# Kernel optimization log

Measured on AMD Instinct MI355X. Metric: run time of the kernel, lower is better.

Reference implementation:

```python
import jax, jax.numpy as jnp
import numpy as np

DIM, HEADS, DIM_HEAD = 1024, 16, 64
INNER = HEADS * DIM_HEAD  # 1024
FF = 4 * DIM
EPS = 1e-5


def layer_norm(x, g, b):
    mu = jnp.mean(x, axis=-1, keepdims=True)
    var = jnp.mean(jnp.square(x - mu), axis=-1, keepdims=True)
    return (x - mu) * jax.lax.rsqrt(var + EPS) * g + b


def setup_inputs() -> dict:
    key = jax.random.key(0)
    ks = jax.random.split(key, 8)
    B, N = 2, 2048
    s = 0.02
    return {
        "x": jax.random.normal(ks[0], (B, N, DIM), dtype=jnp.float32),
        "ln1_g": jnp.ones((DIM,), jnp.float32),
        "ln1_b": jnp.zeros((DIM,), jnp.float32),
        "ln2_g": jnp.ones((DIM,), jnp.float32),
        "ln2_b": jnp.zeros((DIM,), jnp.float32),
        "w_qkv": jax.random.normal(ks[1], (DIM, 3 * INNER), jnp.float32) * s,
        "w_out": jax.random.normal(ks[2], (INNER, DIM), jnp.float32) * s,
        "b_out": jnp.zeros((DIM,), jnp.float32),
        "w_ff1": jax.random.normal(ks[3], (DIM, FF), jnp.float32) * s,
        "b_ff1": jnp.zeros((FF,), jnp.float32),
        "w_ff2": jax.random.normal(ks[4], (FF, DIM), jnp.float32) * s,
        "b_ff2": jnp.zeros((DIM,), jnp.float32),
    }


def reference(x, ln1_g, ln1_b, ln2_g, ln2_b, w_qkv, w_out, b_out,
              w_ff1, b_ff1, w_ff2, b_ff2):
    B, N, _ = x.shape
    scale = DIM_HEAD ** -0.5
    h = layer_norm(x, ln1_g, ln1_b)
    qkv = h @ w_qkv  # [B, N, 3*INNER]
    q, k, v = jnp.split(qkv, 3, axis=-1)
    # b n (h d) -> b h n d
    def to_heads(t):
        return t.reshape(B, N, HEADS, DIM_HEAD).transpose(0, 2, 1, 3)
    q, k, v = to_heads(q), to_heads(k), to_heads(v)
    dots = jnp.einsum('bhnd,bhmd->bhnm', q, k) * scale
    attn = jax.nn.softmax(dots, axis=-1)  # dropout = identity (eval)
    out = jnp.einsum('bhnm,bhmd->bhnd', attn, v)
    out = out.transpose(0, 2, 1, 3).reshape(B, N, INNER)
    out = out @ w_out + b_out
    x = x + out  # residual
    h2 = layer_norm(x, ln2_g, ln2_b)
    ff = jax.nn.gelu(h2 @ w_ff1 + b_ff1, approximate=False) @ w_ff2 + b_ff2
    return x + ff
```

## Files before the change

### kernel.cpp

```cpp
#include <hip/hip_runtime.h>
#include <hip/hip_bf16.h>
#include <math.h>

#define SEQ   2048
#define BATCH 2
#define NROWS 4096
#define DIMM  1024
#define QKV3  3072
#define FFD   4096
#define NHEAD 16
#define DHEAD 64

typedef __bf16 bf16;
typedef __bf16 bf16x4 __attribute__((ext_vector_type(4)));
typedef __bf16 bf16x8 __attribute__((ext_vector_type(8)));
typedef float  f32x4  __attribute__((ext_vector_type(4)));

static __device__ __forceinline__ f32x4 mfma16(bf16x8 a, bf16x8 b, f32x4 c) {
    return __builtin_amdgcn_mfma_f32_16x16x32_bf16(a, b, c, 0, 0, 0);
}

#define GLDS16(gp, lp) __builtin_amdgcn_global_load_lds( \
    (__attribute__((address_space(1))) void*)(gp),       \
    (__attribute__((address_space(3))) void*)(lp), 16, 0, 0)

__global__ __launch_bounds__(256) void tcast_kernel(
    const float* __restrict__ src, bf16* __restrict__ dst, int K, int N)
{
    __shared__ float tile[32][33];
    const int n0 = blockIdx.x * 32;
    const int k0 = blockIdx.y * 32;
    const int r = threadIdx.x >> 5;
    const int c = threadIdx.x & 31;
    #pragma unroll
    for (int i = 0; i < 4; ++i)
        tile[r + 8 * i][c] = src[(size_t)(k0 + r + 8 * i) * N + n0 + c];
    __syncthreads();
    #pragma unroll
    for (int i = 0; i < 4; ++i)
        dst[(size_t)(n0 + r + 8 * i) * K + k0 + c] = (bf16)tile[c][r + 8 * i];
}

__global__ __launch_bounds__(256) void ln_cast_kernel(
    const float* __restrict__ x, const float* __restrict__ g,
    const float* __restrict__ b, bf16* __restrict__ out)
{
    const int row = blockIdx.x;
    const int t = threadIdx.x;
    const float4 v = ((const float4*)(x + (size_t)row * DIMM))[t];
    float s  = v.x + v.y + v.z + v.w;
    float sq = v.x * v.x + v.y * v.y + v.z * v.z + v.w * v.w;
    #pragma unroll
    for (int m = 1; m < 64; m <<= 1) {
        s  += __shfl_xor(s, m, 64);
        sq += __shfl_xor(sq, m, 64);
    }
    __shared__ float ss[4], ssq[4];
    const int wave = t >> 6;
    if ((t & 63) == 0) { ss[wave] = s; ssq[wave] = sq; }
    __syncthreads();
    s  = ss[0] + ss[1] + ss[2] + ss[3];
    sq = ssq[0] + ssq[1] + ssq[2] + ssq[3];
    const float mean = s * (1.0f / DIMM);
    const float var  = sq * (1.0f / DIMM) - mean * mean;
    const float rs   = rsqrtf(var + 1e-5f);
    const float4 gv = ((const float4*)g)[t];
    const float4 bv = ((const float4*)b)[t];
    bf16* o = out + (size_t)row * DIMM + t * 4;
    o[0] = (bf16)((v.x - mean) * rs * gv.x + bv.x);
    o[1] = (bf16)((v.y - mean) * rs * gv.y + bv.y);
    o[2] = (bf16)((v.z - mean) * rs * gv.z + bv.z);
    o[3] = (bf16)((v.w - mean) * rs * gv.w + bv.w);
}

template<int EPI>
__global__ __launch_bounds__(256, 2)
void gemm_bt_kernel(const bf16* __restrict__ A, const bf16* __restrict__ BT,
                    const float* __restrict__ bias, const float* __restrict__ res,
                    void* __restrict__ Cout, int M, int N, int K, int ld)
{
    __shared__ bf16 As[4096];
    __shared__ bf16 Bs[4096];
    const int nb = N >> 7;
    const int chunk = (int)gridDim.x >> 3;
    int idx = (blockIdx.x & 7) * chunk + (blockIdx.x >> 3);
    int ks = 0;
    if (EPI == 3) {
        const int tiles = (M >> 7) * nb;
        ks = idx / tiles;
        idx -= ks * tiles;
    }
    const int bm = idx / nb, bn = idx - bm * nb;
    const int tm = bm << 7, tn = bn << 7;
    const int tid = threadIdx.x;
    const int lane = tid & 63, wave = tid >> 6;
    const int wm = (wave >> 1) << 6, wn = (wave & 1) << 6;
    const int kofs = ks * K;

    const bf16* ga = A  + (size_t)(tm + wave * 32 + (lane >> 2)) * ld + kofs + ((lane & 3) << 3);
    const bf16* gb = BT + (size_t)(tn + wave * 32 + (lane >> 2)) * ld + kofs + ((lane & 3) << 3);
    bf16* la = As + wave * 1024;
    bf16* lb = Bs + wave * 1024;
    const size_t k16 = (size_t)16 * ld;

    f32x4 acc[4][4] = {};
    const int ro = (lane & 15) * 32 + ((lane >> 4) << 3);

    for (int k0 = 0; k0 < K; k0 += 32) {
        __syncthreads();
        GLDS16(ga + k0,       la);
        GLDS16(ga + k0 + k16, la + 512);
        GLDS16(gb + k0,       lb);
        GLDS16(gb + k0 + k16, lb + 512);
        __syncthreads();
        bf16x8 af[4], bfr[4];
        #pragma unroll
        for (int i = 0; i < 4; ++i) {
            af[i]  = *(const bf16x8*)(As + (wm + i * 16) * 32 + ro);
            bfr[i] = *(const bf16x8*)(Bs + (wn + i * 16) * 32 + ro);
        }
        #pragma unroll
        for (int i = 0; i < 4; ++i)
            #pragma unroll
            for (int j = 0; j < 4; ++j)
                acc[i][j] = mfma16(af[i], bfr[j], acc[i][j]);
    }

    const int r0 = tm + wm + ((lane >> 4) << 2);
    const int c0 = tn + wn + (lane & 15);
    if (EPI == 0) {
        bf16* C = (bf16*)Cout;
        #pragma unroll
        for (int i = 0; i < 4; ++i)
            #pragma unroll
            for (int j = 0; j < 4; ++j)
                #pragma unroll
                for (int r = 0; r < 4; ++r)
                    C[(size_t)(r0 + i * 16 + r) * N + (c0 + j * 16)] = (bf16)acc[i][j][r];
    } else if (EPI == 1) {
        float* C = (float*)Cout;
        #pragma unroll
        for (int j = 0; j < 4; ++j) {
            const float bv = bias[c0 + j * 16];
            #pragma unroll
            for (int i = 0; i < 4; ++i)
                #pragma unroll
                for (int r = 0; r < 4; ++r) {
                    const size_t idx2 = (size_t)(r0 + i * 16 + r) * N + (c0 + j * 16);
                    C[idx2] = acc[i][j][r] + bv + res[idx2];
                }
        }
    } else if (EPI == 2) {
        bf16* C = (bf16*)Cout;
        #pragma unroll
        for (int j = 0; j < 4; ++j) {
            const float bv = bias[c0 + j * 16];
            #pragma unroll
            for (int i = 0; i < 4; ++i)
                #pragma unroll
                for (int r = 0; r < 4; ++r) {
                    const float v = acc[i][j][r] + bv;
                    const float gl = 0.5f * v * (1.0f + erff(v * 0.70710678118654752f));
                    C[(size_t)(r0 + i * 16 + r) * N + (c0 + j * 16)] = (bf16)gl;
                }
        }
    } else {
        float* C = (float*)(ks == 0 ? Cout : (void*)res);
        #pragma unroll
        for (int j = 0; j < 4; ++j)
            #pragma unroll
            for (int i = 0; i < 4; ++i)
                #pragma unroll
                for (int r = 0; r < 4; ++r)
                    C[(size_t)(r0 + i * 16 + r) * N + (c0 + j * 16)] = acc[i][j][r];
    }
}

__global__ __launch_bounds__(256) void ff2_reduce_kernel(
    const float* __restrict__ p0, const float* __restrict__ p1,
    const float* __restrict__ bias, const float* __restrict__ res,
    float* __restrict__ out)
{
    const int i = blockIdx.x * 256 + threadIdx.x;
    const float4 a = ((const float4*)p0)[i];
    const float4 b = ((const float4*)p1)[i];
    const float4 r = ((const float4*)res)[i];
    const float4 g = ((const float4*)bias)[i & 255];
    float4 o;
    o.x = a.x + b.x + r.x + g.x;
    o.y = a.y + b.y + r.y + g.y;
    o.z = a.z + b.z + r.z + g.z;
    o.w = a.w + b.w + r.w + g.w;
    ((float4*)out)[i] = o;
}

__global__ __launch_bounds__(256) void vtrans_kernel(
    const bf16* __restrict__ qkv, bf16* __restrict__ vT)
{
    __shared__ bf16 t[64 * 64];
    const int n0 = blockIdx.x * 64;
    const int bh = blockIdx.y;
    const int b = bh >> 4, h = bh & 15;
    const bf16* src = qkv + (size_t)(b * SEQ + n0) * QKV3 + 2 * DIMM + h * DHEAD;

    #pragma unroll
    for (int it = 0; it < 2; ++it) {
        const int c = it * 256 + threadIdx.x;
        const int n = c >> 3, d8 = (c & 7) * 8;
        const bf16x8 v8 = *(const bf16x8*)(src + (size_t)n * QKV3 + d8);
        const int byte = (n * 128 + d8 * 2) ^ (((n >> 3) & 7) << 4);
        *(bf16x8*)((char*)t + byte) = v8;
    }
    __syncthreads();
    #pragma unroll
    for (int it = 0; it < 2; ++it) {
        const int c = it * 256 + threadIdx.x;
        const int d = c >> 3, nc = c & 7;
        bf16x8 o8;
        #pragma unroll
        for (int i = 0; i < 8; ++i) {
            const int n = nc * 8 + i;
            const int byte = (n * 128 + d * 2) ^ ((nc & 7) << 4);
            o8[i] = *(const bf16*)((const char*)t + byte);
        }
        *(bf16x8*)(vT + (size_t)bh * DHEAD * SEQ + (size_t)d * SEQ + n0 + nc * 8) = o8;
    }
}

__global__ __launch_bounds__(256, 4)
void attn_kernel(const bf16* __restrict__ qkv, const bf16* __restrict__ vT,
                 bf16* __restrict__ out)
{
    __shared__ bf16 Ks[2][64 * 64];
    __shared__ bf16 Vs[2][64 * 64];
    __shared__ bf16 Ps[4][16 * 64];
    const int bid = blockIdx.x;
    const int idx = (bid & 7) * 128 + (bid >> 3);
    const int qt = idx & 31;
    const int bh = idx >> 5;
    const int b = bh >> 4, h = bh & 15;
    const int tid = threadIdx.x;
    const int lane = tid & 63, wave = tid >> 6;
    const int q = lane & 15, hi = lane >> 4;

    const bf16* qbase = qkv + (size_t)(b * SEQ) * QKV3 + h * DHEAD;
    const bf16* kbase = qbase + DIMM;
    const bf16* vbase = vT + (size_t)bh * DHEAD * SEQ;

    const int q0 = qt * 64 + wave * 16;
    bf16x8 qf[2];
    {
        const bf16* qp = qbase + (size_t)(q0 + q) * QKV3 + (hi << 3);
        qf[0] = *(const bf16x8*)qp;
        qf[1] = *(const bf16x8*)(qp + 32);
        #pragma unroll
        for (int j = 0; j < 8; ++j) {
            qf[0][j] = (bf16)((float)qf[0][j] * 0.125f);
            qf[1][j] = (bf16)((float)qf[1][j] * 0.125f);
        }
    }

    const int srow = lane >> 3;
    const int scol = ((lane & 7) ^ srow) << 3;
    const bf16* gk = kbase + (size_t)(wave * 16 + srow) * QKV3 + scol;
    const bf16* gv = vbase + (size_t)(wave * 16 + srow) * SEQ + scol;

#define STAGE(BUF, KT) do {                                        \
        bf16* lk_ = &Ks[BUF][wave * 1024];                         \
        bf16* lv_ = &Vs[BUF][wave * 1024];                         \
        GLDS16(gk + (size_t)(KT) * QKV3,       lk_);               \
        GLDS16(gk + (size_t)((KT) + 8) * QKV3, lk_ + 512);         \
        GLDS16(gv + (KT),                      lv_);               \
        GLDS16(gv + (KT) + 8 * SEQ,            lv_ + 512);         \
    } while (0)

    float m = -1e30f, l = 0.0f;
    f32x4 o[4] = {};

    STAGE(0, 0);
    int cur = 0;
    for (int kt = 0; kt < SEQ; kt += 64) {
        __syncthreads();
        if (kt + 64 < SEQ) STAGE(cur ^ 1, kt + 64);

        f32x4 sv[4];
        __builtin_amdgcn_s_setprio(1);
        #pragma unroll
        for (int kf = 0; kf < 4; ++kf) {
            f32x4 z = {0.f, 0.f, 0.f, 0.f};
            sv[kf] = z;
            #pragma unroll
            for (int ks = 0; ks < 2; ++ks) {
                const int row = kf * 16 + q;
                const int bo = (row * 128 + ks * 64 + (hi << 4)) ^ ((row & 7) << 4);
                const bf16x8 kfrag = *(const bf16x8*)((const char*)&Ks[cur][0] + bo);
                sv[kf] = mfma16(kfrag, qf[ks], sv[kf]);
            }
        }
        __builtin_amdgcn_s_setprio(0);

        float pmax;
        {
            float a = fmaxf(fmaxf(sv[0][0], sv[0][1]), fmaxf(sv[0][2], sv[0][3]));
            float b2 = fmaxf(fmaxf(sv[1][0], sv[1][1]), fmaxf(sv[1][2], sv[1][3]));
            float c = fmaxf(fmaxf(sv[2][0], sv[2][1]), fmaxf(sv[2][2], sv[2][3]));
            float d = fmaxf(fmaxf(sv[3][0], sv[3][1]), fmaxf(sv[3][2], sv[3][3]));
            pmax = fmaxf(fmaxf(a, b2), fmaxf(c, d));
        }
        pmax = fmaxf(pmax, __shfl_xor(pmax, 16, 64));
        pmax = fmaxf(pmax, __shfl_xor(pmax, 32, 64));

        if (__any(pmax - m > 8.0f)) {
            const float nm = fmaxf(m, pmax);
            const float fr = __expf(m - nm);
            l *= fr;
            #pragma unroll
            for (int df = 0; df < 4; ++df) {
                o[df][0] *= fr; o[df][1] *= fr;
                o[df][2] *= fr; o[df][3] *= fr;
            }
            m = nm;
        }

        float rsum = 0.0f;
        #pragma unroll
        for (int kf = 0; kf < 4; ++kf) {
            float p0 = __expf(sv[kf][0] - m);
            float p1 = __expf(sv[kf][1] - m);
            float p2 = __expf(sv[kf][2] - m);
            float p3 = __expf(sv[kf][3] - m);
            rsum += (p0 + p1) + (p2 + p3);
            bf16x4 pk = { (bf16)p0, (bf16)p1, (bf16)p2, (bf16)p3 };
            const int bo = (q * 128 + kf * 32 + hi * 8) ^ ((q & 7) << 4);
            *(bf16x4*)((char*)Ps[wave] + bo) = pk;
        }
        rsum += __shfl_xor(rsum, 16, 64);
        rsum += __shfl_xor(rsum, 32, 64);
        l += rsum;

        bf16x8 pf[2];
        #pragma unroll
        for (int ks = 0; ks < 2; ++ks) {
            const int bo = (q * 128 + ks * 64 + (hi << 4)) ^ ((q & 7) << 4);
            pf[ks] = *(const bf16x8*)((const char*)Ps[wave] + bo);
        }
        __builtin_amdgcn_s_setprio(1);
        #pragma unroll
        for (int df = 0; df < 4; ++df)
            #pragma unroll
            for (int ks = 0; ks < 2; ++ks) {
                const int rowv = df * 16 + q;
                const int bo = (rowv * 128 + ks * 64 + (hi << 4)) ^ ((rowv & 7) << 4);
                const bf16x8 vfrag = *(const bf16x8*)((const char*)&Vs[cur][0] + bo);
                o[df] = mfma16(vfrag, pf[ks], o[df]);
            }
        __builtin_amdgcn_s_setprio(0);
        cur ^= 1;
    }
#undef STAGE

    {
        const float inv = 1.0f / l;
        const int grow = b * SEQ + q0 + q;
        #pragma unroll
        for (int df = 0; df < 4; ++df) {
            bf16x4 pk = { (bf16)(o[df][0] * inv), (bf16)(o[df][1] * inv),
                          (bf16)(o[df][2] * inv), (bf16)(o[df][3] * inv) };
            *(bf16x4*)(out + (size_t)grow * DIMM + h * DHEAD + df * 16 + hi * 4) = pk;
        }
    }
}

extern "C" void kernel_launch(void* const* d_in, const int* in_sizes, int n_in,
                              void* d_out, int out_size, void* d_ws, size_t ws_size,
                              hipStream_t stream)
{
    (void)in_sizes; (void)n_in; (void)out_size;
    const float* x    = (const float*)d_in[0];
    const float* ln1g = (const float*)d_in[1];
    const float* ln1b = (const float*)d_in[2];
    const float* ln2g = (const float*)d_in[3];
    const float* ln2b = (const float*)d_in[4];
    const float* wqkv = (const float*)d_in[5];
    const float* wout = (const float*)d_in[6];
    const float* bout = (const float*)d_in[7];
    const float* wff1 = (const float*)d_in[8];
    const float* bff1 = (const float*)d_in[9];
    const float* wff2 = (const float*)d_in[10];
    const float* bff2 = (const float*)d_in[11];

    char* ws = (char*)d_ws;
    const dim3 blk(256);
    const bool splitk = ws_size >= 92274688ULL;

    if (splitk) {
        bf16*  wff2T = (bf16*)(ws);
        bf16*  woutT = (bf16*)(ws + 8388608);
        bf16*  wff1T = (bf16*)(ws + 10485760);
        bf16*  wqkvT = (bf16*)(ws + 18874368);
        bf16*  hbuf  = (bf16*)(ws + 25165824);
        bf16*  qkvb  = (bf16*)(ws + 33554432);
        bf16*  vT    = (bf16*)(ws + 58720256);
        bf16*  attnb = (bf16*)(ws + 67108864);
        float* x2    = (float*)(ws + 75497472);
        bf16*  fbuf  = (bf16*)(ws + 41943040);
        float* p0    = (float*)(ws + 8388608);
        float* p1    = (float*)(ws + 25165824);

        tcast_kernel<<<dim3(QKV3 / 32, DIMM / 32), blk, 0, stream>>>(wqkv, wqkvT, DIMM, QKV3);
        tcast_kernel<<<dim3(DIMM / 32, DIMM / 32), blk, 0, stream>>>(wout, woutT, DIMM, DIMM);
        tcast_kernel<<<dim3(FFD  / 32, DIMM / 32), blk, 0, stream>>>(wff1, wff1T, DIMM, FFD);
        tcast_kernel<<<dim3(DIMM / 32, FFD  / 32), blk, 0, stream>>>(wff2, wff2T, FFD, DIMM);

        ln_cast_kernel<<<NROWS, blk, 0, stream>>>(x, ln1g, ln1b, hbuf);
        gemm_bt_kernel<0><<<(NROWS / 128) * (QKV3 / 128), blk, 0, stream>>>(
            hbuf, wqkvT, nullptr, nullptr, qkvb, NROWS, QKV3, DIMM, DIMM);
        vtrans_kernel<<<dim3(SEQ / 64, BATCH * NHEAD), blk, 0, stream>>>(qkvb, vT);
        attn_kernel<<<dim3(1024), blk, 0, stream>>>(qkvb, vT, attnb);
        gemm_bt_kernel<1><<<(NROWS / 128) * (DIMM / 128), blk, 0, stream>>>(
            attnb, woutT, bout, x, x2, NROWS, DIMM, DIMM, DIMM);
        ln_cast_kernel<<<NROWS, blk, 0, stream>>>(x2, ln2g, ln2b, hbuf);
        gemm_bt_kernel<2><<<(NROWS / 128) * (FFD / 128), blk, 0, stream>>>(
            hbuf, wff1T, bff1, nullptr, fbuf, NROWS, FFD, DIMM, DIMM);
        gemm_bt_kernel<3><<<2 * (NROWS / 128) * (DIMM / 128), blk, 0, stream>>>(
            fbuf, wff2T, nullptr, (const float*)p1, p0, NROWS, DIMM, FFD / 2, FFD);
        ff2_reduce_kernel<<<(NROWS * DIMM) / 1024, blk, 0, stream>>>(
            p0, p1, bff2, x2, (float*)d_out);
    } else {
        bf16*  wqkvT = (bf16*)(ws);
        bf16*  woutT = (bf16*)(ws + 6291456);
        bf16*  wff1T = (bf16*)(ws + 8388608);
        bf16*  wff2T = (bf16*)(ws + 16777216);
        float* x2    = (float*)(ws + 25165824);
        bf16*  vT    = (bf16*)(ws + 25165824);
        bf16*  hbuf  = (bf16*)(ws + 41943040);
        bf16*  qkvb  = (bf16*)(ws + 50331648);
        bf16*  attnb = (bf16*)(ws + 75497472);
        bf16*  fbuf  = (bf16*)(ws + 50331648);

        tcast_kernel<<<dim3(QKV3 / 32, DIMM / 32), blk, 0, stream>>>(wqkv, wqkvT, DIMM, QKV3);
        tcast_kernel<<<dim3(DIMM / 32, DIMM / 32), blk, 0, stream>>>(wout, woutT, DIMM, DIMM);
        tcast_kernel<<<dim3(FFD  / 32, DIMM / 32), blk, 0, stream>>>(wff1, wff1T, DIMM, FFD);
        tcast_kernel<<<dim3(DIMM / 32, FFD  / 32), blk, 0, stream>>>(wff2, wff2T, FFD, DIMM);

        ln_cast_kernel<<<NROWS, blk, 0, stream>>>(x, ln1g, ln1b, hbuf);
        gemm_bt_kernel<0><<<(NROWS / 128) * (QKV3 / 128), blk, 0, stream>>>(
            hbuf, wqkvT, nullptr, nullptr, qkvb, NROWS, QKV3, DIMM, DIMM);
        vtrans_kernel<<<dim3(SEQ / 64, BATCH * NHEAD), blk, 0, stream>>>(qkvb, vT);
        attn_kernel<<<dim3(1024), blk, 0, stream>>>(qkvb, vT, attnb);
        gemm_bt_kernel<1><<<(NROWS / 128) * (DIMM / 128), blk, 0, stream>>>(
            attnb, woutT, bout, x, x2, NROWS, DIMM, DIMM, DIMM);
        ln_cast_kernel<<<NROWS, blk, 0, stream>>>(x2, ln2g, ln2b, hbuf);
        gemm_bt_kernel<2><<<(NROWS / 128) * (FFD / 128), blk, 0, stream>>>(
            hbuf, wff1T, bff1, nullptr, fbuf, NROWS, FFD, DIMM, DIMM);
        gemm_bt_kernel<1><<<(NROWS / 128) * (DIMM / 128), blk, 0, stream>>>(
            fbuf, wff2T, bff2, x2, (float*)d_out, NROWS, DIMM, FFD, FFD);
    }
}
```

Baseline: 274.5 us.

## Double-buffer GEMM LDS tiles and switch attention softmax to exp2 domain

The GEMM kernel gets two LDS buffers so the global-to-LDS load of the next K slice is issued before the MFMAs on the current slice, with one barrier per iteration instead of two. Launch bounds go from 2 to 4 blocks per CU, which limits registers per thread. In attention, the log2(e) factor is folded into the Q scaling so softmax can use exp2f directly, and the lazy-rescale threshold is raised to match base 2. The single-barrier double buffer relies on the async LDS loads completing by the next barrier. The tighter register budget may cause spills.

```diff
diff --git a/kernel.cpp b/kernel.cpp
--- a/kernel.cpp
+++ b/kernel.cpp
@@ -74,13 +74,13 @@
 }
 
 template<int EPI>
-__global__ __launch_bounds__(256, 2)
+__global__ __launch_bounds__(256, 4)
 void gemm_bt_kernel(const bf16* __restrict__ A, const bf16* __restrict__ BT,
                     const float* __restrict__ bias, const float* __restrict__ res,
                     void* __restrict__ Cout, int M, int N, int K, int ld)
 {
-    __shared__ bf16 As[4096];
-    __shared__ bf16 Bs[4096];
+    __shared__ bf16 As[2][4096];
+    __shared__ bf16 Bs[2][4096];
     const int nb = N >> 7;
     const int chunk = (int)gridDim.x >> 3;
     int idx = (blockIdx.x & 7) * chunk + (blockIdx.x >> 3);
@@ -99,32 +99,39 @@
 
     const bf16* ga = A  + (size_t)(tm + wave * 32 + (lane >> 2)) * ld + kofs + ((lane & 3) << 3);
     const bf16* gb = BT + (size_t)(tn + wave * 32 + (lane >> 2)) * ld + kofs + ((lane & 3) << 3);
-    bf16* la = As + wave * 1024;
-    bf16* lb = Bs + wave * 1024;
     const size_t k16 = (size_t)16 * ld;
 
     f32x4 acc[4][4] = {};
     const int ro = (lane & 15) * 32 + ((lane >> 4) << 3);
 
+#define GSTAGE(BUF, KO) do {                          \
+        bf16* la_ = &As[BUF][wave * 1024];            \
+        bf16* lb_ = &Bs[BUF][wave * 1024];            \
+        GLDS16(ga + (KO),       la_);                 \
+        GLDS16(ga + (KO) + k16, la_ + 512);           \
+        GLDS16(gb + (KO),       lb_);                 \
+        GLDS16(gb + (KO) + k16, lb_ + 512);           \
+    } while (0)
+
+    GSTAGE(0, 0);
+    int cur = 0;
     for (int k0 = 0; k0 < K; k0 += 32) {
         __syncthreads();
-        GLDS16(ga + k0,       la);
-        GLDS16(ga + k0 + k16, la + 512);
-        GLDS16(gb + k0,       lb);
-        GLDS16(gb + k0 + k16, lb + 512);
-        __syncthreads();
+        if (k0 + 32 < K) GSTAGE(cur ^ 1, k0 + 32);
         bf16x8 af[4], bfr[4];
         #pragma unroll
         for (int i = 0; i < 4; ++i) {
-            af[i]  = *(const bf16x8*)(As + (wm + i * 16) * 32 + ro);
-            bfr[i] = *(const bf16x8*)(Bs + (wn + i * 16) * 32 + ro);
+            af[i]  = *(const bf16x8*)(&As[cur][0] + (wm + i * 16) * 32 + ro);
+            bfr[i] = *(const bf16x8*)(&Bs[cur][0] + (wn + i * 16) * 32 + ro);
         }
         #pragma unroll
         for (int i = 0; i < 4; ++i)
             #pragma unroll
             for (int j = 0; j < 4; ++j)
                 acc[i][j] = mfma16(af[i], bfr[j], acc[i][j]);
-    }
+        cur ^= 1;
+    }
+#undef GSTAGE
 
     const int r0 = tm + wm + ((lane >> 4) << 2);
     const int c0 = tn + wn + (lane & 15);
@@ -250,13 +257,14 @@
     const int q0 = qt * 64 + wave * 16;
     bf16x8 qf[2];
     {
+        const float qs = 0.125f * 1.4426950408889634f;
         const bf16* qp = qbase + (size_t)(q0 + q) * QKV3 + (hi << 3);
         qf[0] = *(const bf16x8*)qp;
         qf[1] = *(const bf16x8*)(qp + 32);
         #pragma unroll
         for (int j = 0; j < 8; ++j) {
-            qf[0][j] = (bf16)((float)qf[0][j] * 0.125f);
-            qf[1][j] = (bf16)((float)qf[1][j] * 0.125f);
+            qf[0][j] = (bf16)((float)qf[0][j] * qs);
+            qf[1][j] = (bf16)((float)qf[1][j] * qs);
         }
     }
 
@@ -310,9 +318,9 @@
         pmax = fmaxf(pmax, __shfl_xor(pmax, 16, 64));
         pmax = fmaxf(pmax, __shfl_xor(pmax, 32, 64));
 
-        if (__any(pmax - m > 8.0f)) {
+        if (__any(pmax - m > 11.5f)) {
             const float nm = fmaxf(m, pmax);
-            const float fr = __expf(m - nm);
+            const float fr = exp2f(m - nm);
             l *= fr;
             #pragma unroll
             for (int df = 0; df < 4; ++df) {
@@ -325,10 +333,10 @@
         float rsum = 0.0f;
         #pragma unroll
         for (int kf = 0; kf < 4; ++kf) {
-            float p0 = __expf(sv[kf][0] - m);
-            float p1 = __expf(sv[kf][1] - m);
-            float p2 = __expf(sv[kf][2] - m);
-            float p3 = __expf(sv[kf][3] - m);
+            float p0 = exp2f(sv[kf][0] - m);
+            float p1 = exp2f(sv[kf][1] - m);
+            float p2 = exp2f(sv[kf][2] - m);
+            float p3 = exp2f(sv[kf][3] - m);
             rsum += (p0 + p1) + (p2 + p3);
             bf16x4 pk = { (bf16)p0, (bf16)p1, (bf16)p2, (bf16)p3 };
             const int bo = (q * 128 + kf * 32 + hi * 8) ^ ((q & 7) << 4);
```

Measured after the change: 286.8 us. +4.5%, slower.
